# Kernel optimization log

Hardware: AMD Instinct MI355X
Metric: run time of the kernel (lower is better)

The kernel has to match this reference:

```python
import jax, jax.numpy as jnp
import numpy as np

N_NODES = 50000
N_EDGES = 600000
IN_F, HID, OUT_F = 602, 128, 41


def _gconv(x, W, b, src, dst, n):
    # DGL GraphConv, norm='both': D_dst^{-1/2} A (D_src^{-1/2} x W) + b
    ones = jnp.ones(src.shape, dtype=x.dtype)
    deg_out = jnp.clip(jax.ops.segment_sum(ones, src, num_segments=n), 1.0)
    deg_in = jnp.clip(jax.ops.segment_sum(ones, dst, num_segments=n), 1.0)
    h = x * jax.lax.rsqrt(deg_out)[:, None]
    h = h @ W  # dense transform first (in_feats > out_feats path)
    agg = jax.ops.segment_sum(h[src], dst, num_segments=n)  # [N, out]
    return agg * jax.lax.rsqrt(deg_in)[:, None] + b


def setup_inputs() -> dict:
    key = jax.random.key(0)
    ks = jax.random.split(key, 8)
    features = jax.random.normal(ks[0], (N_NODES, IN_F), dtype=jnp.float32)
    src = jax.random.randint(ks[1], (N_EDGES,), 0, N_NODES, dtype=jnp.int32)
    dst = jax.random.randint(ks[2], (N_EDGES,), 0, N_NODES, dtype=jnp.int32)
    def glorot(k, fan_in, fan_out):
        s = jnp.sqrt(6.0 / (fan_in + fan_out)).astype(jnp.float32)
        return jax.random.uniform(k, (fan_in, fan_out), jnp.float32, -s, s)
    return {
        'features': features, 'src': src, 'dst': dst,
        'W1': glorot(ks[3], IN_F, HID), 'b1': jnp.zeros((HID,), jnp.float32),
        'W2': glorot(ks[4], HID, HID), 'b2': jnp.zeros((HID,), jnp.float32),
        'W3': glorot(ks[5], HID, HID), 'b3': jnp.zeros((HID,), jnp.float32),
        'Wfc': glorot(ks[6], HID, OUT_F), 'bfc': jnp.zeros((OUT_F,), jnp.float32),
    }


def reference(features, src, dst, W1, b1, W2, b2, W3, b3, Wfc, bfc):
    n = features.shape[0]
    relu = jax.nn.relu
    x = relu(_gconv(features, W1, b1, src, dst, n))  # x = _x
    _x = relu(_gconv(x, W2, b2, src, dst, n))        # branch (layer2)
    x = relu(_gconv(x, W2, b2, src, dst, n))         # main (same layer2)
    x = relu(_gconv(x, W3, b3, src, dst, n))         # layer3
    x = relu(x + _x)                                  # residual + relu
    return x @ Wfc + bfc
```

## Files before the change

### kernel.cpp

```cpp
#include <hip/hip_runtime.h>
#include <hip/hip_bf16.h>

#define NN   50000
#define NE   600000
#define INF  602
#define HID  128
#define OUTF 41
#define NBLK 196

typedef __attribute__((ext_vector_type(8))) short bf16x8;
typedef __attribute__((ext_vector_type(4))) float f32x4;

__device__ inline unsigned short f2bf(float x) {
    unsigned u = __float_as_uint(x);
    unsigned r = u + 0x7FFF + ((u >> 16) & 1);
    return (unsigned short)(r >> 16);
}

#define GLL16(gp, lp) \
    __builtin_amdgcn_global_load_lds((const __attribute__((address_space(1))) unsigned int*)(gp), \
                                     (__attribute__((address_space(3))) unsigned int*)(lp), 16, 0, 0)

__global__ __launch_bounds__(256) void deg_hist_k(const int* __restrict__ src,
                                                  const int* __restrict__ dst,
                                                  int* __restrict__ cnt_out,
                                                  int* __restrict__ cnt_in, int E) {
    int e = blockIdx.x * 256 + threadIdx.x;
    if (e < E) {
        atomicAdd(&cnt_out[src[e]], 1);
        atomicAdd(&cnt_in[dst[e]], 1);
    }
}

__global__ __launch_bounds__(256) void scan1_k(const int* __restrict__ cnt,
                                               int* __restrict__ rowptr,
                                               int* __restrict__ blockSum) {
    __shared__ int tmp[256];
    int tid = threadIdx.x;
    int i = blockIdx.x * 256 + tid;
    int v = (i < NN) ? cnt[i] : 0;
    tmp[tid] = v;
    __syncthreads();
#pragma unroll
    for (int off = 1; off < 256; off <<= 1) {
        int t = (tid >= off) ? tmp[tid - off] : 0;
        __syncthreads();
        tmp[tid] += t;
        __syncthreads();
    }
    if (i < NN) rowptr[i] = tmp[tid] - v;
    if (tid == 255) blockSum[blockIdx.x] = tmp[255];
}

__global__ __launch_bounds__(256) void scan2_k(const int* __restrict__ blockSum,
                                               int* __restrict__ blockOff,
                                               int* __restrict__ rowptr) {
    __shared__ int tmp[256];
    int tid = threadIdx.x;
    int v = (tid < NBLK) ? blockSum[tid] : 0;
    tmp[tid] = v;
    __syncthreads();
#pragma unroll
    for (int off = 1; off < 256; off <<= 1) {
        int t = (tid >= off) ? tmp[tid - off] : 0;
        __syncthreads();
        tmp[tid] += t;
        __syncthreads();
    }
    if (tid < NBLK) blockOff[tid] = tmp[tid] - v;
    if (tid == 255) rowptr[NN] = tmp[255];
}

__global__ __launch_bounds__(256) void scan3_k(int* __restrict__ rowptr,
                                               const int* __restrict__ blockOff,
                                               int* __restrict__ wcur,
                                               const int* __restrict__ cnt_out,
                                               const int* __restrict__ cnt_in,
                                               float* __restrict__ rs_out,
                                               float* __restrict__ rs_in) {
    int i = blockIdx.x * 256 + threadIdx.x;
    if (i < NN) {
        int r = rowptr[i] + blockOff[blockIdx.x];
        rowptr[i] = r;
        wcur[i] = r;
        int co = cnt_out[i]; if (co < 1) co = 1;
        int ci = cnt_in[i];  if (ci < 1) ci = 1;
        rs_out[i] = rsqrtf((float)co);
        rs_in[i]  = rsqrtf((float)ci);
    }
}

__global__ __launch_bounds__(256) void fill_csr_k(const int* __restrict__ src,
                                                  const int* __restrict__ dst,
                                                  int* __restrict__ wcur,
                                                  int* __restrict__ csrsrc, int E) {
    int e = blockIdx.x * 256 + threadIdx.x;
    if (e < E) {
        int p = atomicAdd(&wcur[dst[e]], 1);
        csrsrc[p] = src[e];
    }
}

__global__ __launch_bounds__(256) void prep_w_k(const float* __restrict__ W, int K,
                                                unsigned short* __restrict__ out, int total4) {
    int i = blockIdx.x * 256 + threadIdx.x;
    if (i >= total4) return;
    int col = i & 127;
    int k4 = (i >> 7) << 2;
    short4 h;
    h.x = (short)f2bf((k4 + 0 < K) ? W[(size_t)(k4 + 0) * HID + col] : 0.f);
    h.y = (short)f2bf((k4 + 1 < K) ? W[(size_t)(k4 + 1) * HID + col] : 0.f);
    h.z = (short)f2bf((k4 + 2 < K) ? W[(size_t)(k4 + 2) * HID + col] : 0.f);
    h.w = (short)f2bf((k4 + 3 < K) ? W[(size_t)(k4 + 3) * HID + col] : 0.f);
    *(short4*)&out[(size_t)(k4 >> 3) * 1024 + col * 8 + (k4 & 7)] = h;
}

__global__ __launch_bounds__(256) void gemm1_k(const float* __restrict__ A,
                                               const unsigned short* __restrict__ Wt,
                                               const float* __restrict__ rs_out,
                                               unsigned short* __restrict__ H, int n) {
    __shared__ __attribute__((aligned(16))) short As[64 * 136];
    __shared__ __attribute__((aligned(16))) short Bs[16 * 1024];

    const int tid = threadIdx.x;
    const int wave = tid >> 6;
    const int lane = tid & 63;
    const int quad = lane >> 4;
    const int l16 = lane & 15;
    const int rowBase = blockIdx.x * 64;
    const int tileBase = rowBase + wave * 16;

    float4 apf[8];
    auto loadA = [&](int ch) {
        int kb = ch * 128;
#pragma unroll
        for (int c = 0; c < 8; ++c) {
            int f = c * 256 + tid;
            int row = f >> 5;
            int kc = (f & 31) << 2;
            int grow = rowBase + row;
            int gk = kb + kc;
            float4 v = {0.f, 0.f, 0.f, 0.f};
            if (grow < n) {
                if (gk + 3 < INF) {
                    v = *(const float4*)(A + (size_t)grow * INF + gk);
                } else {
                    if (gk + 0 < INF) v.x = A[(size_t)grow * INF + gk + 0];
                    if (gk + 1 < INF) v.y = A[(size_t)grow * INF + gk + 1];
                    if (gk + 2 < INF) v.z = A[(size_t)grow * INF + gk + 2];
                }
            }
            apf[c] = v;
        }
    };
    auto storeA = [&]() {
#pragma unroll
        for (int c = 0; c < 8; ++c) {
            int f = c * 256 + tid;
            int row = f >> 5;
            int kc = (f & 31) << 2;
            short4 h;
            h.x = (short)f2bf(apf[c].x); h.y = (short)f2bf(apf[c].y);
            h.z = (short)f2bf(apf[c].z); h.w = (short)f2bf(apf[c].w);
            *(short4*)&As[row * 136 + kc] = h;
        }
    };
    auto issueB = [&](int ch) {
#pragma unroll
        for (int c = 0; c < 8; ++c)
            GLL16(Wt + (size_t)ch * 16384 + c * 2048 + tid * 8, &Bs[c * 2048 + tid * 8]);
    };

    f32x4 acc[8];
#pragma unroll
    for (int j = 0; j < 8; ++j) acc[j] = (f32x4){0.f, 0.f, 0.f, 0.f};

    loadA(0);
    for (int ch = 0; ch < 5; ++ch) {
        __syncthreads();
        issueB(ch);
        storeA();
        __syncthreads();
        if (ch + 1 < 5) loadA(ch + 1);
#pragma unroll
        for (int s = 0; s < 4; ++s) {
            bf16x8 af = *(const bf16x8*)&As[(wave * 16 + l16) * 136 + s * 32 + quad * 8];
            const short* bg = &Bs[(s * 4 + quad) * 1024 + l16 * 8];
#pragma unroll
            for (int nt = 0; nt < 8; ++nt) {
                bf16x8 bf = *(const bf16x8*)(bg + nt * 128);
                acc[nt] = __builtin_amdgcn_mfma_f32_16x16x32_bf16(af, bf, acc[nt], 0, 0, 0);
            }
        }
    }

#pragma unroll
    for (int r = 0; r < 4; ++r) {
        int row = tileBase + quad * 4 + r;
        if (row < n) {
            float ro = rs_out[row];
#pragma unroll
            for (int nt = 0; nt < 8; ++nt)
                H[(size_t)row * HID + nt * 16 + l16] = f2bf(acc[nt][r] * ro);
        }
    }
}

__global__ __launch_bounds__(256) void gemm_hid_k(const unsigned short* __restrict__ A,
                                                  const unsigned short* __restrict__ Wt,
                                                  unsigned short* __restrict__ H, int n) {
    __shared__ __attribute__((aligned(16))) short As[64 * 136];
    __shared__ __attribute__((aligned(16))) short Bs[16384];

    const int tid = threadIdx.x;
    const int wave = tid >> 6;
    const int lane = tid & 63;
    const int quad = lane >> 4;
    const int l16 = lane & 15;
    const int wm = wave >> 1;
    const int wn = wave & 1;
    const int rowBase = blockIdx.x * 64;

#pragma unroll
    for (int c = 0; c < 8; ++c)
        GLL16(Wt + c * 2048 + tid * 8, &Bs[c * 2048 + tid * 8]);

#pragma unroll
    for (int c = 0; c < 4; ++c) {
        int f = c * 256 + tid;
        int row = f >> 4;
        int k16 = (f & 15) << 3;
        int grow = rowBase + row;
        int4 v = {0, 0, 0, 0};
        if (grow < n) v = *(const int4*)(A + (size_t)grow * HID + k16);
        *(int4*)&As[row * 136 + k16] = v;
    }
    __syncthreads();

    f32x4 acc[2][4];
#pragma unroll
    for (int i = 0; i < 2; ++i)
#pragma unroll
        for (int j = 0; j < 4; ++j) acc[i][j] = (f32x4){0.f, 0.f, 0.f, 0.f};

#pragma unroll
    for (int kq = 0; kq < 4; ++kq) {
        bf16x8 af[2], bfr[4];
#pragma unroll
        for (int mt = 0; mt < 2; ++mt)
            af[mt] = *(const bf16x8*)&As[(wm * 32 + mt * 16 + l16) * 136 + kq * 32 + quad * 8];
#pragma unroll
        for (int nt = 0; nt < 4; ++nt)
            bfr[nt] = *(const bf16x8*)&Bs[(kq * 4 + quad) * 1024 + (wn * 64 + nt * 16 + l16) * 8];
#pragma unroll
        for (int mt = 0; mt < 2; ++mt)
#pragma unroll
            for (int nt = 0; nt < 4; ++nt)
                acc[mt][nt] = __builtin_amdgcn_mfma_f32_16x16x32_bf16(af[mt], bfr[nt], acc[mt][nt], 0, 0, 0);
    }

#pragma unroll
    for (int mt = 0; mt < 2; ++mt)
#pragma unroll
        for (int r = 0; r < 4; ++r) {
            int row = rowBase + wm * 32 + mt * 16 + quad * 4 + r;
            if (row < n) {
#pragma unroll
                for (int nt = 0; nt < 4; ++nt) {
                    int col = wn * 64 + nt * 16 + l16;
                    H[(size_t)row * HID + col] = f2bf(acc[mt][nt][r]);
                }
            }
        }
}

__global__ __launch_bounds__(256) void gather_k(const unsigned short* __restrict__ H,
                                                const int* __restrict__ rowptr,
                                                const int* __restrict__ csrsrc,
                                                const float* __restrict__ rs_in,
                                                const float* __restrict__ rs_out,
                                                const float* __restrict__ bias,
                                                const float* __restrict__ resid,
                                                float* __restrict__ outX,
                                                unsigned short* __restrict__ outXs,
                                                int n) {
    int node = blockIdx.x * 4 + (threadIdx.x >> 6);
    if (node >= n) return;
    int lane = threadIdx.x & 63;
    const unsigned int* Hu = (const unsigned int*)H;
    int beg = rowptr[node], end = rowptr[node + 1];
    float ax = 0.f, ay = 0.f, bx2 = 0.f, by2 = 0.f;
    int p = beg;
    for (; p + 1 < end; p += 2) {
        unsigned u0 = Hu[(size_t)csrsrc[p] * 64 + lane];
        unsigned u1 = Hu[(size_t)csrsrc[p + 1] * 64 + lane];
        ax += __uint_as_float(u0 << 16);
        ay += __uint_as_float(u0 & 0xFFFF0000u);
        bx2 += __uint_as_float(u1 << 16);
        by2 += __uint_as_float(u1 & 0xFFFF0000u);
    }
    if (p < end) {
        unsigned u = Hu[(size_t)csrsrc[p] * 64 + lane];
        ax += __uint_as_float(u << 16);
        ay += __uint_as_float(u & 0xFFFF0000u);
    }
    ax += bx2; ay += by2;
    float ri = rs_in[node];
    float vx = fmaxf(ax * ri + bias[lane * 2], 0.f);
    float vy = fmaxf(ay * ri + bias[lane * 2 + 1], 0.f);
    if (resid) {
        float2 r = *(const float2*)(resid + (size_t)node * HID + lane * 2);
        vx = fmaxf(vx + r.x, 0.f);
        vy = fmaxf(vy + r.y, 0.f);
    }
    size_t o = (size_t)node * HID + lane * 2;
    if (outX) { *(float2*)(outX + o) = make_float2(vx, vy); }
    if (outXs) {
        float ro = rs_out[node];
        ushort2 h;
        h.x = f2bf(vx * ro);
        h.y = f2bf(vy * ro);
        *(ushort2*)(outXs + o) = h;
    }
}

__global__ __launch_bounds__(256) void fc_k(const float* __restrict__ X,
                                            const float* __restrict__ Wfc,
                                            const float* __restrict__ bfc,
                                            float* __restrict__ out, int n) {
    __shared__ float Ws[HID * OUTF];
    __shared__ float Xs[4][HID];
    int tid = threadIdx.x;
    for (int i = tid; i < HID * OUTF; i += 256) Ws[i] = Wfc[i];
    int rowBase = blockIdx.x * 4;
    for (int i = tid; i < 4 * HID; i += 256) {
        int r = i >> 7, c = i & 127;
        int gr = rowBase + r;
        Xs[r][c] = (gr < n) ? X[(size_t)gr * HID + c] : 0.f;
    }
    __syncthreads();
    int wv = tid >> 6, lane = tid & 63;
    int row = rowBase + wv;
    if (row < n && lane < OUTF) {
        float acc = bfc[lane];
#pragma unroll 8
        for (int k = 0; k < HID; ++k) acc += Xs[wv][k] * Ws[k * OUTF + lane];
        out[(size_t)row * OUTF + lane] = acc;
    }
}

extern "C" void kernel_launch(void* const* d_in, const int* in_sizes, int n_in,
                              void* d_out, int out_size, void* d_ws, size_t ws_size,
                              hipStream_t stream) {
    const float* feat = (const float*)d_in[0];
    const int* src = (const int*)d_in[1];
    const int* dst = (const int*)d_in[2];
    const float* W1 = (const float*)d_in[3];
    const float* b1 = (const float*)d_in[4];
    const float* W2 = (const float*)d_in[5];
    const float* b2 = (const float*)d_in[6];
    const float* W3 = (const float*)d_in[7];
    const float* b3 = (const float*)d_in[8];
    const float* Wfc = (const float*)d_in[9];
    const float* bfc = (const float*)d_in[10];
    float* out = (float*)d_out;

    char* w = (char*)d_ws;
    auto alloc = [&](size_t b) -> void* {
        void* p = (void*)w;
        w += (b + 255) & ~(size_t)255;
        return p;
    };
    int* cnt_out = (int*)alloc(NN * sizeof(int));
    int* cnt_in  = (int*)alloc(NN * sizeof(int));
    int* rowptr  = (int*)alloc((NN + 1) * sizeof(int));
    int* wcur    = (int*)alloc(NN * sizeof(int));
    int* csrsrc  = (int*)alloc(NE * sizeof(int));
    int* blockSum = (int*)alloc(NBLK * sizeof(int));
    int* blockOff = (int*)alloc(NBLK * sizeof(int));
    float* rs_out = (float*)alloc(NN * sizeof(float));
    float* rs_in  = (float*)alloc(NN * sizeof(float));
    unsigned short* W1t = (unsigned short*)alloc(10 * 8192 * sizeof(unsigned short));
    unsigned short* W2t = (unsigned short*)alloc(16384 * sizeof(unsigned short));
    unsigned short* W3t = (unsigned short*)alloc(16384 * sizeof(unsigned short));
    unsigned short* Hb = (unsigned short*)alloc((size_t)NN * HID * sizeof(unsigned short));
    unsigned short* Xb = (unsigned short*)alloc((size_t)NN * HID * sizeof(unsigned short));
    float* resid = (float*)alloc((size_t)NN * HID * sizeof(float));
    float* Xfc   = (float*)alloc((size_t)NN * HID * sizeof(float));

    hipMemsetAsync(cnt_out, 0, NN * sizeof(int), stream);
    hipMemsetAsync(cnt_in, 0, NN * sizeof(int), stream);

    prep_w_k<<<80, 256, 0, stream>>>(W1, INF, W1t, 20480);
    prep_w_k<<<16, 256, 0, stream>>>(W2, HID, W2t, 4096);
    prep_w_k<<<16, 256, 0, stream>>>(W3, HID, W3t, 4096);

    deg_hist_k<<<(NE + 255) / 256, 256, 0, stream>>>(src, dst, cnt_out, cnt_in, NE);
    scan1_k<<<NBLK, 256, 0, stream>>>(cnt_in, rowptr, blockSum);
    scan2_k<<<1, 256, 0, stream>>>(blockSum, blockOff, rowptr);
    scan3_k<<<NBLK, 256, 0, stream>>>(rowptr, blockOff, wcur, cnt_out, cnt_in, rs_out, rs_in);
    fill_csr_k<<<(NE + 255) / 256, 256, 0, stream>>>(src, dst, wcur, csrsrc, NE);

    const int gblk = (NN + 63) / 64;
    gemm1_k<<<gblk, 256, 0, stream>>>(feat, W1t, rs_out, Hb, NN);
    gather_k<<<(NN + 3) / 4, 256, 0, stream>>>(Hb, rowptr, csrsrc, rs_in, rs_out, b1,
                                               nullptr, nullptr, Xb, NN);
    gemm_hid_k<<<gblk, 256, 0, stream>>>(Xb, W2t, Hb, NN);
    gather_k<<<(NN + 3) / 4, 256, 0, stream>>>(Hb, rowptr, csrsrc, rs_in, rs_out, b2,
                                               nullptr, resid, Xb, NN);
    gemm_hid_k<<<gblk, 256, 0, stream>>>(Xb, W3t, Hb, NN);
    gather_k<<<(NN + 3) / 4, 256, 0, stream>>>(Hb, rowptr, csrsrc, rs_in, rs_out, b3,
                                               resid, Xfc, nullptr, NN);
    fc_k<<<(NN + 3) / 4, 256, 0, stream>>>(Xfc, Wfc, bfc, out, NN);
}
```

Measured before the change: 513.4 us.

## Gather four nodes per wave with 16-byte row loads and shuffled indices

The CSR gather kernel now assigns four destination nodes per wavefront, with 16 lanes each loading 8 bf16 features (int4) per neighbor row. Neighbor indices are loaded cooperatively and broadcast via shuffles, and four rows are loaded in flight per step to raise memory-level parallelism. The epilogue is vectorised to float4/int4 stores. Separately, the two degree-count memsets are merged and the W2/W3 weight-prep launches are fused into one kernel to cut launch overhead. Lanes in a wave may diverge when the four nodes have different degrees.

```diff
diff --git a/kernel.cpp b/kernel.cpp
--- a/kernel.cpp
+++ b/kernel.cpp
@@ -101,9 +101,8 @@
     }
 }
 
-__global__ __launch_bounds__(256) void prep_w_k(const float* __restrict__ W, int K,
-                                                unsigned short* __restrict__ out, int total4) {
-    int i = blockIdx.x * 256 + threadIdx.x;
+__device__ inline void prep_w_body(const float* __restrict__ W, int K,
+                                   unsigned short* __restrict__ out, int total4, int i) {
     if (i >= total4) return;
     int col = i & 127;
     int k4 = (i >> 7) << 2;
@@ -113,6 +112,21 @@
     h.z = (short)f2bf((k4 + 2 < K) ? W[(size_t)(k4 + 2) * HID + col] : 0.f);
     h.w = (short)f2bf((k4 + 3 < K) ? W[(size_t)(k4 + 3) * HID + col] : 0.f);
     *(short4*)&out[(size_t)(k4 >> 3) * 1024 + col * 8 + (k4 & 7)] = h;
+}
+
+__global__ __launch_bounds__(256) void prep_w_k(const float* __restrict__ W, int K,
+                                                unsigned short* __restrict__ out, int total4) {
+    prep_w_body(W, K, out, total4, blockIdx.x * 256 + threadIdx.x);
+}
+
+__global__ __launch_bounds__(256) void prep_w2_k(const float* __restrict__ Wa,
+                                                 unsigned short* __restrict__ outa,
+                                                 const float* __restrict__ Wb,
+                                                 unsigned short* __restrict__ outb) {
+    if (blockIdx.x < 16)
+        prep_w_body(Wa, HID, outa, 4096, blockIdx.x * 256 + threadIdx.x);
+    else
+        prep_w_body(Wb, HID, outb, 4096, (blockIdx.x - 16) * 256 + threadIdx.x);
 }
 
 __global__ __launch_bounds__(256) void gemm1_k(const float* __restrict__ A,
@@ -284,43 +298,88 @@
                                                 float* __restrict__ outX,
                                                 unsigned short* __restrict__ outXs,
                                                 int n) {
-    int node = blockIdx.x * 4 + (threadIdx.x >> 6);
-    if (node >= n) return;
-    int lane = threadIdx.x & 63;
-    const unsigned int* Hu = (const unsigned int*)H;
-    int beg = rowptr[node], end = rowptr[node + 1];
-    float ax = 0.f, ay = 0.f, bx2 = 0.f, by2 = 0.f;
-    int p = beg;
-    for (; p + 1 < end; p += 2) {
-        unsigned u0 = Hu[(size_t)csrsrc[p] * 64 + lane];
-        unsigned u1 = Hu[(size_t)csrsrc[p + 1] * 64 + lane];
-        ax += __uint_as_float(u0 << 16);
-        ay += __uint_as_float(u0 & 0xFFFF0000u);
-        bx2 += __uint_as_float(u1 << 16);
-        by2 += __uint_as_float(u1 & 0xFFFF0000u);
-    }
-    if (p < end) {
-        unsigned u = Hu[(size_t)csrsrc[p] * 64 + lane];
-        ax += __uint_as_float(u << 16);
-        ay += __uint_as_float(u & 0xFFFF0000u);
-    }
-    ax += bx2; ay += by2;
+    const int lane = threadIdx.x & 63;
+    const int g = lane >> 4;
+    const int l = lane & 15;
+    const int gbase = g << 4;
+    const int wid = blockIdx.x * 4 + (threadIdx.x >> 6);
+    const int node = wid * 4 + g;
+    const bool alive = node < n;
+
+    int beg = 0, end = 0;
+    if (alive) { beg = rowptr[node]; end = rowptr[node + 1]; }
+
+    float acc[8];
+#pragma unroll
+    for (int k = 0; k < 8; ++k) acc[k] = 0.f;
+
+    auto accum = [&](int s) {
+        int4 u = *(const int4*)(H + (size_t)s * HID + l * 8);
+        unsigned x = (unsigned)u.x, y = (unsigned)u.y, z = (unsigned)u.z, w = (unsigned)u.w;
+        acc[0] += __uint_as_float(x << 16); acc[1] += __uint_as_float(x & 0xFFFF0000u);
+        acc[2] += __uint_as_float(y << 16); acc[3] += __uint_as_float(y & 0xFFFF0000u);
+        acc[4] += __uint_as_float(z << 16); acc[5] += __uint_as_float(z & 0xFFFF0000u);
+        acc[6] += __uint_as_float(w << 16); acc[7] += __uint_as_float(w & 0xFFFF0000u);
+    };
+
+    for (int base = beg; base < end; base += 16) {
+        int m = end - base; if (m > 16) m = 16;
+        int idx = (l < m) ? csrsrc[base + l] : 0;
+        int j = 0;
+        for (; j + 3 < m; j += 4) {
+            int s0 = __shfl(idx, gbase | j);
+            int s1 = __shfl(idx, gbase | (j + 1));
+            int s2 = __shfl(idx, gbase | (j + 2));
+            int s3 = __shfl(idx, gbase | (j + 3));
+            int4 u0 = *(const int4*)(H + (size_t)s0 * HID + l * 8);
+            int4 u1 = *(const int4*)(H + (size_t)s1 * HID + l * 8);
+            int4 u2 = *(const int4*)(H + (size_t)s2 * HID + l * 8);
+            int4 u3 = *(const int4*)(H + (size_t)s3 * HID + l * 8);
+#pragma unroll
+            for (int q = 0; q < 4; ++q) {
+                int4 u = (q == 0) ? u0 : (q == 1) ? u1 : (q == 2) ? u2 : u3;
+                unsigned x = (unsigned)u.x, y = (unsigned)u.y, z = (unsigned)u.z, w = (unsigned)u.w;
+                acc[0] += __uint_as_float(x << 16); acc[1] += __uint_as_float(x & 0xFFFF0000u);
+                acc[2] += __uint_as_float(y << 16); acc[3] += __uint_as_float(y & 0xFFFF0000u);
+                acc[4] += __uint_as_float(z << 16); acc[5] += __uint_as_float(z & 0xFFFF0000u);
+                acc[6] += __uint_as_float(w << 16); acc[7] += __uint_as_float(w & 0xFFFF0000u);
+            }
+        }
+        for (; j < m; ++j) accum(__shfl(idx, gbase | j));
+    }
+
+    if (!alive) return;
+
     float ri = rs_in[node];
-    float vx = fmaxf(ax * ri + bias[lane * 2], 0.f);
-    float vy = fmaxf(ay * ri + bias[lane * 2 + 1], 0.f);
+    float4 b0 = *(const float4*)(bias + l * 8);
+    float4 b1 = *(const float4*)(bias + l * 8 + 4);
+    float v[8];
+    v[0] = fmaxf(acc[0] * ri + b0.x, 0.f); v[1] = fmaxf(acc[1] * ri + b0.y, 0.f);
+    v[2] = fmaxf(acc[2] * ri + b0.z, 0.f); v[3] = fmaxf(acc[3] * ri + b0.w, 0.f);
+    v[4] = fmaxf(acc[4] * ri + b1.x, 0.f); v[5] = fmaxf(acc[5] * ri + b1.y, 0.f);
+    v[6] = fmaxf(acc[6] * ri + b1.z, 0.f); v[7] = fmaxf(acc[7] * ri + b1.w, 0.f);
+
+    size_t o = (size_t)node * HID + l * 8;
     if (resid) {
-        float2 r = *(const float2*)(resid + (size_t)node * HID + lane * 2);
-        vx = fmaxf(vx + r.x, 0.f);
-        vy = fmaxf(vy + r.y, 0.f);
-    }
-    size_t o = (size_t)node * HID + lane * 2;
-    if (outX) { *(float2*)(outX + o) = make_float2(vx, vy); }
+        float4 r0 = *(const float4*)(resid + o);
+        float4 r1 = *(const float4*)(resid + o + 4);
+        v[0] = fmaxf(v[0] + r0.x, 0.f); v[1] = fmaxf(v[1] + r0.y, 0.f);
+        v[2] = fmaxf(v[2] + r0.z, 0.f); v[3] = fmaxf(v[3] + r0.w, 0.f);
+        v[4] = fmaxf(v[4] + r1.x, 0.f); v[5] = fmaxf(v[5] + r1.y, 0.f);
+        v[6] = fmaxf(v[6] + r1.z, 0.f); v[7] = fmaxf(v[7] + r1.w, 0.f);
+    }
+    if (outX) {
+        *(float4*)(outX + o) = make_float4(v[0], v[1], v[2], v[3]);
+        *(float4*)(outX + o + 4) = make_float4(v[4], v[5], v[6], v[7]);
+    }
     if (outXs) {
         float ro = rs_out[node];
-        ushort2 h;
-        h.x = f2bf(vx * ro);
-        h.y = f2bf(vy * ro);
-        *(ushort2*)(outXs + o) = h;
+        int4 h;
+        h.x = (int)(((unsigned)f2bf(v[1] * ro) << 16) | f2bf(v[0] * ro));
+        h.y = (int)(((unsigned)f2bf(v[3] * ro) << 16) | f2bf(v[2] * ro));
+        h.z = (int)(((unsigned)f2bf(v[5] * ro) << 16) | f2bf(v[4] * ro));
+        h.w = (int)(((unsigned)f2bf(v[7] * ro) << 16) | f2bf(v[6] * ro));
+        *(int4*)(outXs + o) = h;
     }
 }
 
@@ -371,8 +430,9 @@
         w += (b + 255) & ~(size_t)255;
         return p;
     };
-    int* cnt_out = (int*)alloc(NN * sizeof(int));
-    int* cnt_in  = (int*)alloc(NN * sizeof(int));
+    int* cnt = (int*)alloc(2 * NN * sizeof(int));
+    int* cnt_out = cnt;
+    int* cnt_in  = cnt + NN;
     int* rowptr  = (int*)alloc((NN + 1) * sizeof(int));
     int* wcur    = (int*)alloc(NN * sizeof(int));
     int* csrsrc  = (int*)alloc(NE * sizeof(int));
@@ -388,12 +448,10 @@
     float* resid = (float*)alloc((size_t)NN * HID * sizeof(float));
     float* Xfc   = (float*)alloc((size_t)NN * HID * sizeof(float));
 
-    hipMemsetAsync(cnt_out, 0, NN * sizeof(int), stream);
-    hipMemsetAsync(cnt_in, 0, NN * sizeof(int), stream);
+    hipMemsetAsync(cnt, 0, 2 * NN * sizeof(int), stream);
 
     prep_w_k<<<80, 256, 0, stream>>>(W1, INF, W1t, 20480);
-    prep_w_k<<<16, 256, 0, stream>>>(W2, HID, W2t, 4096);
-    prep_w_k<<<16, 256, 0, stream>>>(W3, HID, W3t, 4096);
+    prep_w2_k<<<32, 256, 0, stream>>>(W2, W2t, W3, W3t);
 
     deg_hist_k<<<(NE + 255) / 256, 256, 0, stream>>>(src, dst, cnt_out, cnt_in, NE);
     scan1_k<<<NBLK, 256, 0, stream>>>(cnt_in, rowptr, blockSum);
@@ -402,14 +460,15 @@
     fill_csr_k<<<(NE + 255) / 256, 256, 0, stream>>>(src, dst, wcur, csrsrc, NE);
 
     const int gblk = (NN + 63) / 64;
+    const int ablk = (NN + 15) / 16;
     gemm1_k<<<gblk, 256, 0, stream>>>(feat, W1t, rs_out, Hb, NN);
-    gather_k<<<(NN + 3) / 4, 256, 0, stream>>>(Hb, rowptr, csrsrc, rs_in, rs_out, b1,
-                                               nullptr, nullptr, Xb, NN);
+    gather_k<<<ablk, 256, 0, stream>>>(Hb, rowptr, csrsrc, rs_in, rs_out, b1,
+                                       nullptr, nullptr, Xb, NN);
     gemm_hid_k<<<gblk, 256, 0, stream>>>(Xb, W2t, Hb, NN);
-    gather_k<<<(NN + 3) / 4, 256, 0, stream>>>(Hb, rowptr, csrsrc, rs_in, rs_out, b2,
-                                               nullptr, resid, Xb, NN);
+    gather_k<<<ablk, 256, 0, stream>>>(Hb, rowptr, csrsrc, rs_in, rs_out, b2,
+                                       nullptr, resid, Xb, NN);
     gemm_hid_k<<<gblk, 256, 0, stream>>>(Xb, W3t, Hb, NN);
-    gather_k<<<(NN + 3) / 4, 256, 0, stream>>>(Hb, rowptr, csrsrc, rs_in, rs_out, b3,
-                                               resid, Xfc, nullptr, NN);
+    gather_k<<<ablk, 256, 0, stream>>>(Hb, rowptr, csrsrc, rs_in, rs_out, b3,
+                                       resid, Xfc, nullptr, NN);
     fc_k<<<(NN + 3) / 4, 256, 0, stream>>>(Xfc, Wfc, bfc, out, NN);
 }
```

After: 455.7 us. 11.2% less time.

## Rewrite gather as XCD-aware column-sliced kernel and merge setup kernels

Applied to the files above, without the earlier changes.

Replaces the per-node wave gather with a persistent kernel in which each block handles a node chunk and a 32-column slice, with the slice chosen from the block index modulo 8. The intent is that blocks on the same XCD touch the same column slice of H, so that slice fits and stays in that XCD's L2. The kernel also batches neighbour indices through shuffles and uses nontemporal stores. Separately, the two memsets and three weight-prep kernels become one kernel, and scan2/scan3 are merged by having each block reduce the block sums itself. The risks are that the XCD placement is assumed rather than guaranteed, and that narrower 8-byte loads per lane cost extra memory traffic.

```diff
diff --git a/kernel.cpp b/kernel.cpp
--- a/kernel.cpp
+++ b/kernel.cpp
@@ -8,8 +8,14 @@
 #define OUTF 41
 #define NBLK 196
 
+#define GXCD   128
+#define GBLKS  (8 * GXCD)
+#define GCHUNKS (2 * GXCD)
+#define GCHN   ((NN + GCHUNKS - 1) / GCHUNKS)
+
 typedef __attribute__((ext_vector_type(8))) short bf16x8;
 typedef __attribute__((ext_vector_type(4))) float f32x4;
+typedef __attribute__((ext_vector_type(2))) int i32x2;
 
 __device__ inline unsigned short f2bf(float x) {
     unsigned u = __float_as_uint(x);
@@ -52,35 +58,30 @@
     if (tid == 255) blockSum[blockIdx.x] = tmp[255];
 }
 
-__global__ __launch_bounds__(256) void scan2_k(const int* __restrict__ blockSum,
-                                               int* __restrict__ blockOff,
-                                               int* __restrict__ rowptr) {
-    __shared__ int tmp[256];
-    int tid = threadIdx.x;
-    int v = (tid < NBLK) ? blockSum[tid] : 0;
-    tmp[tid] = v;
+__global__ __launch_bounds__(256) void scan23_k(int* __restrict__ rowptr,
+                                                const int* __restrict__ blockSum,
+                                                int* __restrict__ wcur,
+                                                const int* __restrict__ cnt_out,
+                                                const int* __restrict__ cnt_in,
+                                                float* __restrict__ rs_out,
+                                                float* __restrict__ rs_in) {
+    const int tid = threadIdx.x;
+    const int bid = blockIdx.x;
+    int vAll = (tid < NBLK) ? blockSum[tid] : 0;
+    int vPre = (tid < bid) ? vAll : 0;
+#pragma unroll
+    for (int o = 32; o; o >>= 1) {
+        vAll += __shfl_down(vAll, o);
+        vPre += __shfl_down(vPre, o);
+    }
+    __shared__ int sA[4], sP[4];
+    if ((tid & 63) == 0) { sA[tid >> 6] = vAll; sP[tid >> 6] = vPre; }
     __syncthreads();
-#pragma unroll
-    for (int off = 1; off < 256; off <<= 1) {
-        int t = (tid >= off) ? tmp[tid - off] : 0;
-        __syncthreads();
-        tmp[tid] += t;
-        __syncthreads();
-    }
-    if (tid < NBLK) blockOff[tid] = tmp[tid] - v;
-    if (tid == 255) rowptr[NN] = tmp[255];
-}
-
-__global__ __launch_bounds__(256) void scan3_k(int* __restrict__ rowptr,
-                                               const int* __restrict__ blockOff,
-                                               int* __restrict__ wcur,
-                                               const int* __restrict__ cnt_out,
-                                               const int* __restrict__ cnt_in,
-                                               float* __restrict__ rs_out,
-                                               float* __restrict__ rs_in) {
-    int i = blockIdx.x * 256 + threadIdx.x;
+    int offAll = sA[0] + sA[1] + sA[2] + sA[3];
+    int offPre = sP[0] + sP[1] + sP[2] + sP[3];
+    int i = bid * 256 + tid;
     if (i < NN) {
-        int r = rowptr[i] + blockOff[blockIdx.x];
+        int r = rowptr[i] + offPre;
         rowptr[i] = r;
         wcur[i] = r;
         int co = cnt_out[i]; if (co < 1) co = 1;
@@ -88,6 +89,7 @@
         rs_out[i] = rsqrtf((float)co);
         rs_in[i]  = rsqrtf((float)ci);
     }
+    if (bid == NBLK - 1 && tid == 0) rowptr[NN] = offAll;
 }
 
 __global__ __launch_bounds__(256) void fill_csr_k(const int* __restrict__ src,
@@ -101,9 +103,8 @@
     }
 }
 
-__global__ __launch_bounds__(256) void prep_w_k(const float* __restrict__ W, int K,
-                                                unsigned short* __restrict__ out, int total4) {
-    int i = blockIdx.x * 256 + threadIdx.x;
+__device__ inline void prep_w_body(const float* __restrict__ W, int K,
+                                   unsigned short* __restrict__ out, int total4, int i) {
     if (i >= total4) return;
     int col = i & 127;
     int k4 = (i >> 7) << 2;
@@ -113,6 +114,25 @@
     h.z = (short)f2bf((k4 + 2 < K) ? W[(size_t)(k4 + 2) * HID + col] : 0.f);
     h.w = (short)f2bf((k4 + 3 < K) ? W[(size_t)(k4 + 3) * HID + col] : 0.f);
     *(short4*)&out[(size_t)(k4 >> 3) * 1024 + col * 8 + (k4 & 7)] = h;
+}
+
+__global__ __launch_bounds__(256) void prep_all_k(const float* __restrict__ W1,
+                                                  const float* __restrict__ W2,
+                                                  const float* __restrict__ W3,
+                                                  unsigned short* __restrict__ W1t,
+                                                  unsigned short* __restrict__ W2t,
+                                                  unsigned short* __restrict__ W3t,
+                                                  int* __restrict__ cnt) {
+    int b = blockIdx.x;
+    if (b < 80) {
+        int t = b * 256 + threadIdx.x;
+        prep_w_body(W1, INF, W1t, 20480, t);
+        for (int i = t; i < 2 * NN; i += 20480) cnt[i] = 0;
+    } else if (b < 96) {
+        prep_w_body(W2, HID, W2t, 4096, (b - 80) * 256 + threadIdx.x);
+    } else {
+        prep_w_body(W3, HID, W3t, 4096, (b - 96) * 256 + threadIdx.x);
+    }
 }
 
 __global__ __launch_bounds__(256) void gemm1_k(const float* __restrict__ A,
@@ -274,53 +294,98 @@
         }
 }
 
-__global__ __launch_bounds__(256) void gather_k(const unsigned short* __restrict__ H,
-                                                const int* __restrict__ rowptr,
-                                                const int* __restrict__ csrsrc,
-                                                const float* __restrict__ rs_in,
-                                                const float* __restrict__ rs_out,
-                                                const float* __restrict__ bias,
-                                                const float* __restrict__ resid,
-                                                float* __restrict__ outX,
-                                                unsigned short* __restrict__ outXs,
-                                                int n) {
-    int node = blockIdx.x * 4 + (threadIdx.x >> 6);
-    if (node >= n) return;
-    int lane = threadIdx.x & 63;
-    const unsigned int* Hu = (const unsigned int*)H;
-    int beg = rowptr[node], end = rowptr[node + 1];
-    float ax = 0.f, ay = 0.f, bx2 = 0.f, by2 = 0.f;
-    int p = beg;
-    for (; p + 1 < end; p += 2) {
-        unsigned u0 = Hu[(size_t)csrsrc[p] * 64 + lane];
-        unsigned u1 = Hu[(size_t)csrsrc[p + 1] * 64 + lane];
-        ax += __uint_as_float(u0 << 16);
-        ay += __uint_as_float(u0 & 0xFFFF0000u);
-        bx2 += __uint_as_float(u1 << 16);
-        by2 += __uint_as_float(u1 & 0xFFFF0000u);
-    }
-    if (p < end) {
-        unsigned u = Hu[(size_t)csrsrc[p] * 64 + lane];
-        ax += __uint_as_float(u << 16);
-        ay += __uint_as_float(u & 0xFFFF0000u);
-    }
-    ax += bx2; ay += by2;
-    float ri = rs_in[node];
-    float vx = fmaxf(ax * ri + bias[lane * 2], 0.f);
-    float vy = fmaxf(ay * ri + bias[lane * 2 + 1], 0.f);
-    if (resid) {
-        float2 r = *(const float2*)(resid + (size_t)node * HID + lane * 2);
-        vx = fmaxf(vx + r.x, 0.f);
-        vy = fmaxf(vy + r.y, 0.f);
-    }
-    size_t o = (size_t)node * HID + lane * 2;
-    if (outX) { *(float2*)(outX + o) = make_float2(vx, vy); }
-    if (outXs) {
-        float ro = rs_out[node];
-        ushort2 h;
-        h.x = f2bf(vx * ro);
-        h.y = f2bf(vy * ro);
-        *(ushort2*)(outXs + o) = h;
+__global__ __launch_bounds__(256) void gath_slice_k(const unsigned short* __restrict__ Hin,
+                                                    const int* __restrict__ rowptr,
+                                                    const int* __restrict__ csrsrc,
+                                                    const float* __restrict__ rs_in,
+                                                    const float* __restrict__ rs_out,
+                                                    const float* __restrict__ bias,
+                                                    const float* __restrict__ residIn,
+                                                    float* __restrict__ residOut,
+                                                    unsigned short* __restrict__ outXs,
+                                                    float* __restrict__ outX,
+                                                    int n) {
+    const int b = blockIdx.x;
+    const int xcd = b & 7;
+    const int slice = xcd >> 1;
+    const int chunk = ((b >> 3) << 1) + (xcd & 1);
+    const int n0 = chunk * GCHN;
+    const int n1 = min(n0 + GCHN, n);
+
+    const int tid = threadIdx.x;
+    const int wave = tid >> 6;
+    const int lane = tid & 63;
+    const int g = lane >> 3;
+    const int l8 = lane & 7;
+    const int gbase = g << 3;
+    const int col = slice * 32 + l8 * 4;
+
+    const float4 bb = *(const float4*)(bias + col);
+
+    for (int nb = n0 + wave * 8; nb < n1; nb += 32) {
+        int node = nb + g;
+        bool alive = node < n1;
+        int beg = 0, end = 0;
+        if (alive) { beg = rowptr[node]; end = rowptr[node + 1]; }
+
+        float a0 = 0.f, a1 = 0.f, a2 = 0.f, a3 = 0.f;
+
+        for (int base = beg; base < end; base += 8) {
+            int m = end - base; if (m > 8) m = 8;
+            int idx = (l8 < m) ? csrsrc[base + l8] : 0;
+            int j = 0;
+            for (; j + 3 < m; j += 4) {
+                int s0 = __shfl(idx, gbase | j);
+                int s1 = __shfl(idx, gbase | (j + 1));
+                int s2 = __shfl(idx, gbase | (j + 2));
+                int s3 = __shfl(idx, gbase | (j + 3));
+                int2 u0 = *(const int2*)(Hin + (size_t)s0 * HID + col);
+                int2 u1 = *(const int2*)(Hin + (size_t)s1 * HID + col);
+                int2 u2 = *(const int2*)(Hin + (size_t)s2 * HID + col);
+                int2 u3 = *(const int2*)(Hin + (size_t)s3 * HID + col);
+#pragma unroll
+                for (int q = 0; q < 4; ++q) {
+                    int2 u = (q == 0) ? u0 : (q == 1) ? u1 : (q == 2) ? u2 : u3;
+                    unsigned x = (unsigned)u.x, y = (unsigned)u.y;
+                    a0 += __uint_as_float(x << 16); a1 += __uint_as_float(x & 0xFFFF0000u);
+                    a2 += __uint_as_float(y << 16); a3 += __uint_as_float(y & 0xFFFF0000u);
+                }
+            }
+            for (; j < m; ++j) {
+                int s = __shfl(idx, gbase | j);
+                int2 u = *(const int2*)(Hin + (size_t)s * HID + col);
+                unsigned x = (unsigned)u.x, y = (unsigned)u.y;
+                a0 += __uint_as_float(x << 16); a1 += __uint_as_float(x & 0xFFFF0000u);
+                a2 += __uint_as_float(y << 16); a3 += __uint_as_float(y & 0xFFFF0000u);
+            }
+        }
+
+        if (alive) {
+            float ri = rs_in[node];
+            float v0 = fmaxf(a0 * ri + bb.x, 0.f);
+            float v1 = fmaxf(a1 * ri + bb.y, 0.f);
+            float v2 = fmaxf(a2 * ri + bb.z, 0.f);
+            float v3 = fmaxf(a3 * ri + bb.w, 0.f);
+            size_t o = (size_t)node * HID + col;
+            if (residOut)
+                __builtin_nontemporal_store((f32x4){v0, v1, v2, v3}, (f32x4*)(residOut + o));
+            if (residIn) {
+                f32x4 r = __builtin_nontemporal_load((const f32x4*)(residIn + o));
+                v0 = fmaxf(v0 + r[0], 0.f);
+                v1 = fmaxf(v1 + r[1], 0.f);
+                v2 = fmaxf(v2 + r[2], 0.f);
+                v3 = fmaxf(v3 + r[3], 0.f);
+            }
+            if (outXs) {
+                float ro = rs_out[node];
+                i32x2 h;
+                h[0] = (int)(((unsigned)f2bf(v1 * ro) << 16) | f2bf(v0 * ro));
+                h[1] = (int)(((unsigned)f2bf(v3 * ro) << 16) | f2bf(v2 * ro));
+                __builtin_nontemporal_store(h, (i32x2*)(outXs + o));
+            }
+            if (outX)
+                __builtin_nontemporal_store((f32x4){v0, v1, v2, v3}, (f32x4*)(outX + o));
+        }
     }
 }
 
@@ -371,45 +436,39 @@
         w += (b + 255) & ~(size_t)255;
         return p;
     };
-    int* cnt_out = (int*)alloc(NN * sizeof(int));
-    int* cnt_in  = (int*)alloc(NN * sizeof(int));
+    int* cnt = (int*)alloc(2 * NN * sizeof(int));
+    int* cnt_out = cnt;
+    int* cnt_in  = cnt + NN;
     int* rowptr  = (int*)alloc((NN + 1) * sizeof(int));
     int* wcur    = (int*)alloc(NN * sizeof(int));
     int* csrsrc  = (int*)alloc(NE * sizeof(int));
     int* blockSum = (int*)alloc(NBLK * sizeof(int));
-    int* blockOff = (int*)alloc(NBLK * sizeof(int));
     float* rs_out = (float*)alloc(NN * sizeof(float));
     float* rs_in  = (float*)alloc(NN * sizeof(float));
     unsigned short* W1t = (unsigned short*)alloc(10 * 8192 * sizeof(unsigned short));
     unsigned short* W2t = (unsigned short*)alloc(16384 * sizeof(unsigned short));
     unsigned short* W3t = (unsigned short*)alloc(16384 * sizeof(unsigned short));
+    unsigned short* Ha = (unsigned short*)alloc((size_t)NN * HID * sizeof(unsigned short));
     unsigned short* Hb = (unsigned short*)alloc((size_t)NN * HID * sizeof(unsigned short));
     unsigned short* Xb = (unsigned short*)alloc((size_t)NN * HID * sizeof(unsigned short));
     float* resid = (float*)alloc((size_t)NN * HID * sizeof(float));
     float* Xfc   = (float*)alloc((size_t)NN * HID * sizeof(float));
 
-    hipMemsetAsync(cnt_out, 0, NN * sizeof(int), stream);
-    hipMemsetAsync(cnt_in, 0, NN * sizeof(int), stream);
-
-    prep_w_k<<<80, 256, 0, stream>>>(W1, INF, W1t, 20480);
-    prep_w_k<<<16, 256, 0, stream>>>(W2, HID, W2t, 4096);
-    prep_w_k<<<16, 256, 0, stream>>>(W3, HID, W3t, 4096);
-
+    prep_all_k<<<112, 256, 0, stream>>>(W1, W2, W3, W1t, W2t, W3t, cnt);
     deg_hist_k<<<(NE + 255) / 256, 256, 0, stream>>>(src, dst, cnt_out, cnt_in, NE);
     scan1_k<<<NBLK, 256, 0, stream>>>(cnt_in, rowptr, blockSum);
-    scan2_k<<<1, 256, 0, stream>>>(blockSum, blockOff, rowptr);
-    scan3_k<<<NBLK, 256, 0, stream>>>(rowptr, blockOff, wcur, cnt_out, cnt_in, rs_out, rs_in);
+    scan23_k<<<NBLK, 256, 0, stream>>>(rowptr, blockSum, wcur, cnt_out, cnt_in, rs_out, rs_in);
     fill_csr_k<<<(NE + 255) / 256, 256, 0, stream>>>(src, dst, wcur, csrsrc, NE);
 
     const int gblk = (NN + 63) / 64;
-    gemm1_k<<<gblk, 256, 0, stream>>>(feat, W1t, rs_out, Hb, NN);
-    gather_k<<<(NN + 3) / 4, 256, 0, stream>>>(Hb, rowptr, csrsrc, rs_in, rs_out, b1,
-                                               nullptr, nullptr, Xb, NN);
+    gemm1_k<<<gblk, 256, 0, stream>>>(feat, W1t, rs_out, Ha, NN);
+    gath_slice_k<<<GBLKS, 256, 0, stream>>>(Ha, rowptr, csrsrc, rs_in, rs_out, b1,
+                                            nullptr, nullptr, Xb, nullptr, NN);
     gemm_hid_k<<<gblk, 256, 0, stream>>>(Xb, W2t, Hb, NN);
-    gather_k<<<(NN + 3) / 4, 256, 0, stream>>>(Hb, rowptr, csrsrc, rs_in, rs_out, b2,
-                                               nullptr, resid, Xb, NN);
-    gemm_hid_k<<<gblk, 256, 0, stream>>>(Xb, W3t, Hb, NN);
-    gather_k<<<(NN + 3) / 4, 256, 0, stream>>>(Hb, rowptr, csrsrc, rs_in, rs_out, b3,
-                                               resid, Xfc, nullptr, NN);
+    gath_slice_k<<<GBLKS, 256, 0, stream>>>(Hb, rowptr, csrsrc, rs_in, rs_out, b2,
+                                            nullptr, resid, Xb, nullptr, NN);
+    gemm_hid_k<<<gblk, 256, 0, stream>>>(Xb, W3t, Ha, NN);
+    gath_slice_k<<<GBLKS, 256, 0, stream>>>(Ha, rowptr, csrsrc, rs_in, rs_out, b3,
+                                            resid, nullptr, nullptr, Xfc, NN);
     fc_k<<<(NN + 3) / 4, 256, 0, stream>>>(Xfc, Wfc, bfc, out, NN);
 }
```

Result: no change. 523.4 us (+2.0%).
